# Kernel optimization log

Measured on AMD Instinct MI355X. Metric: run time of the kernel, lower is better.

## Reference

```python
import jax, jax.numpy as jnp
import numpy as np

DIM = 1024
LATENT = 512
HEADS = 16
HEAD_DIM = DIM // HEADS


def setup_inputs() -> dict:
    key = jax.random.key(0)
    ks = jax.random.split(key, 9)
    s = 0.02
    return {
        "x": jax.random.normal(ks[0], (2, 2048, DIM), dtype=jnp.float32),
        "Wq": jax.random.normal(ks[1], (DIM, DIM), dtype=jnp.float32) * s,
        "Wkv": jax.random.normal(ks[2], (DIM, 2 * DIM), dtype=jnp.float32) * s,
        "Wk1": jax.random.normal(ks[3], (DIM, LATENT), dtype=jnp.float32) * s,
        "Wk2": jax.random.normal(ks[4], (LATENT, DIM), dtype=jnp.float32) * s,
        "Wv1": jax.random.normal(ks[5], (DIM, LATENT), dtype=jnp.float32) * s,
        "Wv2": jax.random.normal(ks[6], (LATENT, DIM), dtype=jnp.float32) * s,
        "Wo": jax.random.normal(ks[7], (DIM, DIM), dtype=jnp.float32) * s,
        "bo": jax.random.normal(ks[8], (DIM,), dtype=jnp.float32) * s,
    }


def reference(x, Wq, Wkv, Wk1, Wk2, Wv1, Wv2, Wo, bo):
    b, n, dim = x.shape
    scale = HEAD_DIM ** -0.5
    q = x @ Wq                               # [b, n, dim]
    kv = x @ Wkv                             # [b, n, 2*dim]
    k, v = kv[..., :dim], kv[..., dim:]
    # latent bottleneck MLPs (Linear -> ReLU -> Linear, no bias)
    k = jax.nn.relu(k @ Wk1) @ Wk2           # [b, n, dim]
    v = jax.nn.relu(v @ Wv1) @ Wv2           # [b, n, dim]
    # split heads: [b, n, h*d] -> [b, h, n, d]
    def split_heads(t):
        return t.reshape(b, n, HEADS, HEAD_DIM).transpose(0, 2, 1, 3)
    q = split_heads(q) * scale
    k = split_heads(k)
    v = split_heads(v)
    scores = jnp.einsum('bhid,bhjd->bhij', q, k)   # [b, h, n, n]
    attn = jax.nn.softmax(scores, axis=-1)
    out = jnp.einsum('bhij,bhjd->bhid', attn, v)   # [b, h, n, d]
    out = out.transpose(0, 2, 1, 3).reshape(b, n, dim)
    return out @ Wo + bo
```

## Files before the change

kernel.cpp:

```cpp
#include <hip/hip_runtime.h>
#include <stdint.h>


typedef __attribute__((ext_vector_type(8))) __bf16 bf16x8;
typedef __attribute__((ext_vector_type(4))) float f32x4;

__device__ inline unsigned short f2bfu(float f) {
    __bf16 b = (__bf16)f;
    return __builtin_bit_cast(unsigned short, b);
}

__device__ inline float exp2_fast(float f) {
    return __builtin_amdgcn_exp2f(f);
}

__device__ inline void load_lds16(const void* g, void* l) {
    __builtin_amdgcn_global_load_lds(
        (const __attribute__((address_space(1))) uint32_t*)g,
        (__attribute__((address_space(3))) uint32_t*)l, 16, 0, 0);
}

__device__ inline f32x4 mfma_bf16(bf16x8 a, bf16x8 b, f32x4 c) {
    return __builtin_amdgcn_mfma_f32_16x16x32_bf16(a, b, c, 0, 0, 0);
}

__global__ __launch_bounds__(256) void prep_kernel(
    const float* __restrict__ x, unsigned short* __restrict__ xb,
    const float* __restrict__ Wkv, unsigned short* __restrict__ Wkvb,
    const float* __restrict__ Wq,  const float* __restrict__ Wo,
    const float* __restrict__ Wk1, const float* __restrict__ Wv1,
    const float* __restrict__ Wk2, const float* __restrict__ Wv2,
    unsigned short* __restrict__ WqkvT, unsigned short* __restrict__ WoT,
    unsigned short* __restrict__ Wk1T,  unsigned short* __restrict__ Wv1T,
    unsigned short* __restrict__ Wk2T,  unsigned short* __restrict__ Wv2T,
    float qscale)
{
    __shared__ float tile[64][65];
    int id = blockIdx.x;
    int t = threadIdx.x;

    if (id < 6144) {
        const float* s = (id < 4096) ? x : Wkv;
        unsigned short* d = (id < 4096) ? xb : Wkvb;
        int base = (id < 4096) ? id : (id - 4096);
        int i = (base * 256 + t) * 4;
        float4 v = *(const float4*)&s[i];
        ushort4 o;
        o.x = f2bfu(v.x); o.y = f2bfu(v.y); o.z = f2bfu(v.z); o.w = f2bfu(v.w);
        *(ushort4*)&d[i] = o;
        return;
    }

    int r = id - 6144;
    const float* src; unsigned short* dst; int R, C; float sc; int bx, by;
    if (r < 512) {
        int z = r >> 8; int rr = r & 255; bx = rr & 15; by = rr >> 4;
        src = z ? Wo : Wq; dst = z ? WoT : WqkvT;
        R = 1024; C = 1024; sc = z ? 1.0f : qscale;
    } else if (r < 768) {
        int rr = r - 512; int z = rr >> 7; rr &= 127; bx = rr & 7; by = rr >> 3;
        src = z ? Wv1 : Wk1; dst = z ? Wv1T : Wk1T;
        R = 1024; C = 512; sc = 1.0f;
    } else {
        int rr = r - 768; int z = rr >> 7; rr &= 127; bx = rr & 15; by = rr >> 4;
        src = z ? Wv2 : Wk2; dst = z ? Wv2T : Wk2T;
        R = 512; C = 1024; sc = 1.0f;
    }

    int c0 = bx * 64, r0 = by * 64;
    int col = t & 63, rr4 = t >> 6;
#pragma unroll
    for (int i = 0; i < 16; ++i)
        tile[rr4 + i * 4][col] = src[(size_t)(r0 + rr4 + i * 4) * C + c0 + col];
    __syncthreads();
#pragma unroll
    for (int i = 0; i < 16; ++i) {
        int r2 = rr4 + i * 4;
        dst[(size_t)(c0 + r2) * R + r0 + col] = f2bfu(tile[col][r2] * sc);
    }
}

template<int BN, bool OUTVT = false>
__global__ __launch_bounds__(256) void gemm_bf16_kernel(
    const unsigned short* __restrict__ A0, const unsigned short* __restrict__ A1,
    const unsigned short* __restrict__ B0, const unsigned short* __restrict__ B1,
    void* __restrict__ C0, void* __restrict__ C1,
    int lda, int ldb, int ldc, int K,
    const float* __restrict__ bias, int relu, int out_f32)
{
    const unsigned short* A = blockIdx.z ? A1 : A0;
    const unsigned short* Bt = blockIdx.z ? B1 : B0;
    void* C = blockIdx.z ? C1 : C0;

    constexpr int NI = BN / 32;
    constexpr int AH = 128 * 32;
    constexpr int BH = BN * 32;
    __shared__ unsigned short Als[4 * AH];
    __shared__ unsigned short Bls[4 * BH];
    int t = threadIdx.x;
    int lane = t & 63, w = t >> 6;
    int n0 = blockIdx.x * BN, m0 = blockIdx.y * 128;
    int wm = (w & 1) * 64, wn = (w >> 1) * (BN / 2);
    int lrow = lane & 15, quad = lane >> 4;

    f32x4 acc[4][NI];
    f32x4 z = {0.f, 0.f, 0.f, 0.f};
#pragma unroll
    for (int i = 0; i < 4; ++i)
#pragma unroll
        for (int j = 0; j < NI; ++j) acc[i][j] = z;

    int c0 = t, c1 = t + 256;
    const unsigned short* ag0 = A + (size_t)(m0 + (c0 >> 2)) * lda + (c0 & 3) * 8;
    const unsigned short* ag1 = A + (size_t)(m0 + (c1 >> 2)) * lda + (c1 & 3) * 8;
    const unsigned short* bg0 = Bt + (size_t)(n0 + (c0 >> 2)) * ldb + (c0 & 3) * 8;
    const unsigned short* bg1 = Bt + (size_t)(n0 + ((c1 >> 2) & (BN - 1))) * ldb + (c1 & 3) * 8;

    for (int k0 = 0; k0 < K; k0 += 128) {
        __syncthreads();
#pragma unroll
        for (int h = 0; h < 4; ++h) {
            load_lds16(ag0 + k0 + h * 32, &Als[h * AH + c0 * 8]);
            load_lds16(ag1 + k0 + h * 32, &Als[h * AH + c1 * 8]);
            load_lds16(bg0 + k0 + h * 32, &Bls[h * BH + c0 * 8]);
            if constexpr (BN == 128)
                load_lds16(bg1 + k0 + h * 32, &Bls[h * BH + c1 * 8]);
        }
        __syncthreads();

#pragma unroll
        for (int kk = 0; kk < 4; ++kk) {
            bf16x8 af[4], bfr[NI];
#pragma unroll
            for (int mi = 0; mi < 4; ++mi)
                af[mi] = *(const bf16x8*)&Als[kk * AH + (wm + mi * 16 + lrow) * 32 + quad * 8];
#pragma unroll
            for (int ni = 0; ni < NI; ++ni)
                bfr[ni] = *(const bf16x8*)&Bls[kk * BH + (wn + ni * 16 + lrow) * 32 + quad * 8];
#pragma unroll
            for (int mi = 0; mi < 4; ++mi)
#pragma unroll
                for (int ni = 0; ni < NI; ++ni)
                    acc[mi][ni] = mfma_bf16(af[mi], bfr[ni], acc[mi][ni]);
        }
    }

    if (OUTVT && blockIdx.z) {
        int bb = m0 >> 11;
        int npb = (m0 & 2047) + wm;
        unsigned short* vt = (unsigned short*)C;
#pragma unroll
        for (int mi = 0; mi < 4; ++mi)
#pragma unroll
            for (int ni = 0; ni < NI; ++ni) {
                int col = n0 + wn + ni * 16 + lrow;
                int np = npb + mi * 16 + quad * 4;
                ushort4 o;
                o.x = f2bfu(acc[mi][ni][0]);
                o.y = f2bfu(acc[mi][ni][1]);
                o.z = f2bfu(acc[mi][ni][2]);
                o.w = f2bfu(acc[mi][ni][3]);
                *(ushort4*)&vt[(size_t)(bb * 1024 + col) * 2048 + np] = o;
            }
        return;
    }

#pragma unroll
    for (int mi = 0; mi < 4; ++mi)
#pragma unroll
        for (int ni = 0; ni < NI; ++ni)
#pragma unroll
            for (int r = 0; r < 4; ++r) {
                int row = m0 + wm + mi * 16 + quad * 4 + r;
                int col = n0 + wn + ni * 16 + lrow;
                float v = acc[mi][ni][r];
                if (bias) v += bias[col];
                if (relu == 1 || (relu == 2 && col >= 1024)) v = fmaxf(v, 0.0f);
                if (out_f32) ((float*)C)[(size_t)row * ldc + col] = v;
                else ((unsigned short*)C)[(size_t)row * ldc + col] = f2bfu(v);
            }
}

__global__ __launch_bounds__(256, 2) void flash_mfma_kernel(
    const unsigned short* __restrict__ Q, int ldq,
    const unsigned short* __restrict__ K, int ldk,
    const unsigned short* __restrict__ Vt, unsigned short* __restrict__ O)
{
    __shared__ __align__(16) unsigned short Kls[2][2 * 64 * 32];
    __shared__ __align__(16) unsigned short Vls[2][2 * 64 * 32];
    __shared__ __align__(16) unsigned short Pls[4][2][16 * 64];

    int pbid = blockIdx.x;
    int lbid = (pbid >> 3) + (pbid & 7) * 64;
    int q0 = (lbid & 15) * 128, bh = lbid >> 4;
    int b = bh >> 4, h = bh & 15;
    int t = threadIdx.x;
    int lane = t & 63, w = t >> 6;
    int lrow = lane & 15, quad = lane >> 4;

    bf16x8 qf[2][2];
#pragma unroll
    for (int qb = 0; qb < 2; ++qb) {
        const unsigned short* qrow =
            Q + (size_t)(b * 2048 + q0 + w * 32 + qb * 16 + lrow) * ldq + h * 64;
        qf[qb][0] = *(const bf16x8*)&qrow[quad * 8];
        qf[qb][1] = *(const bf16x8*)&qrow[32 + quad * 8];
    }

    f32x4 z = {0.f, 0.f, 0.f, 0.f};
    f32x4 acco[2][4];
    float m_run[2][4], l_run[2][4];
#pragma unroll
    for (int qb = 0; qb < 2; ++qb)
#pragma unroll
        for (int r = 0; r < 4; ++r) {
            acco[qb][r] = z;
            m_run[qb][r] = -1e30f;
            l_run[qb][r] = 0.f;
        }

    int row4 = t >> 2;
    int seg = (t & 3) * 8;
    const unsigned short* kg = K + (size_t)(b * 2048 + row4) * ldk + h * 64 + seg;
    const unsigned short* vg = Vt + (size_t)(bh * 64 + row4) * 2048 + seg;

    char* pb[2] = { (char*)&Pls[w][0][0], (char*)&Pls[w][1][0] };

    load_lds16(kg,      &Kls[0][t * 8]);
    load_lds16(kg + 32, &Kls[0][2048 + t * 8]);
    load_lds16(vg,      &Vls[0][t * 8]);
    load_lds16(vg + 32, &Vls[0][2048 + t * 8]);
    __syncthreads();

    int cur = 0;
    for (int kt = 0; kt < 2048; kt += 64) {
        if (kt + 64 < 2048) {
            const unsigned short* kgk = kg + (size_t)(kt + 64) * ldk;
            const unsigned short* vgk = vg + kt + 64;
            int nb = cur ^ 1;
            load_lds16(kgk,      &Kls[nb][t * 8]);
            load_lds16(kgk + 32, &Kls[nb][2048 + t * 8]);
            load_lds16(vgk,      &Vls[nb][t * 8]);
            load_lds16(vgk + 32, &Vls[nb][2048 + t * 8]);
        }

        f32x4 s[2][4];
        __builtin_amdgcn_s_setprio(1);
#pragma unroll
        for (int kt8 = 0; kt8 < 4; ++kt8) {
            bf16x8 k0 = *(const bf16x8*)&Kls[cur][(kt8 * 16 + lrow) * 32 + quad * 8];
            bf16x8 k1 = *(const bf16x8*)&Kls[cur][2048 + (kt8 * 16 + lrow) * 32 + quad * 8];
            s[0][kt8] = mfma_bf16(qf[0][0], k0, z);
            s[0][kt8] = mfma_bf16(qf[0][1], k1, s[0][kt8]);
            s[1][kt8] = mfma_bf16(qf[1][0], k0, z);
            s[1][kt8] = mfma_bf16(qf[1][1], k1, s[1][kt8]);
        }
        __builtin_amdgcn_s_setprio(0);

#pragma unroll
        for (int qb = 0; qb < 2; ++qb) {
            float pm[4];
#pragma unroll
            for (int r = 0; r < 4; ++r)
                pm[r] = fmaxf(fmaxf(s[qb][0][r], s[qb][1][r]),
                              fmaxf(s[qb][2][r], s[qb][3][r]));
            bool ok = (pm[0] <= m_run[qb][0] + 8.f) && (pm[1] <= m_run[qb][1] + 8.f)
                   && (pm[2] <= m_run[qb][2] + 8.f) && (pm[3] <= m_run[qb][3] + 8.f);
            if (!__all(ok)) {
#pragma unroll
                for (int r = 0; r < 4; ++r) {
#pragma unroll
                    for (int off = 1; off < 16; off <<= 1)
                        pm[r] = fmaxf(pm[r], __shfl_xor(pm[r], off, 64));
                    float mnew = fmaxf(m_run[qb][r], pm[r]);
                    float al = exp2_fast(m_run[qb][r] - mnew);
                    m_run[qb][r] = mnew;
                    l_run[qb][r] *= al;
#pragma unroll
                    for (int nt = 0; nt < 4; ++nt) acco[qb][nt][r] *= al;
                }
            }
#pragma unroll
            for (int kt8 = 0; kt8 < 4; ++kt8)
#pragma unroll
                for (int r = 0; r < 4; ++r) {
                    float p = exp2_fast(s[qb][kt8][r] - m_run[qb][r]);
                    l_run[qb][r] += p;
                    int row = quad * 4 + r;
                    int boff = (row * 128 + (kt8 * 16 + lrow) * 2) ^ ((row & 7) << 4);
                    *(unsigned short*)(pb[qb] + boff) = f2bfu(p);
                }
        }

        __builtin_amdgcn_s_setprio(1);
#pragma unroll
        for (int ks = 0; ks < 2; ++ks) {
            int rb = (lrow * 128 + ks * 64 + quad * 16) ^ ((lrow & 7) << 4);
            bf16x8 pf0 = *(const bf16x8*)(pb[0] + rb);
            bf16x8 pf1 = *(const bf16x8*)(pb[1] + rb);
#pragma unroll
            for (int nt = 0; nt < 4; ++nt) {
                bf16x8 vf = *(const bf16x8*)&Vls[cur][ks * 2048 + (nt * 16 + lrow) * 32 + quad * 8];
                acco[0][nt] = mfma_bf16(pf0, vf, acco[0][nt]);
                acco[1][nt] = mfma_bf16(pf1, vf, acco[1][nt]);
            }
        }
        __builtin_amdgcn_s_setprio(0);

        __syncthreads();
        cur ^= 1;
    }

#pragma unroll
    for (int qb = 0; qb < 2; ++qb)
#pragma unroll
        for (int r = 0; r < 4; ++r) {
            float lr = l_run[qb][r];
#pragma unroll
            for (int off = 1; off < 16; off <<= 1)
                lr += __shfl_xor(lr, off, 64);
            float rl = 1.0f / lr;
            int row = b * 2048 + q0 + w * 32 + qb * 16 + quad * 4 + r;
#pragma unroll
            for (int nt = 0; nt < 4; ++nt)
                O[(size_t)row * 1024 + h * 64 + nt * 16 + lrow] =
                    f2bfu(acco[qb][nt][r] * rl);
        }
}


extern "C" void kernel_launch(void* const* d_in, const int* in_sizes, int n_in,
                              void* d_out, int out_size, void* d_ws, size_t ws_size,
                              hipStream_t stream) {
    const float* x   = (const float*)d_in[0];
    const float* Wq  = (const float*)d_in[1];
    const float* Wkv = (const float*)d_in[2];
    const float* Wk1 = (const float*)d_in[3];
    const float* Wk2 = (const float*)d_in[4];
    const float* Wv1 = (const float*)d_in[5];
    const float* Wv2 = (const float*)d_in[6];
    const float* Wo  = (const float*)d_in[7];
    const float* bo  = (const float*)d_in[8];
    float* out = (float*)d_out;

    unsigned short* p = (unsigned short*)d_ws;
    unsigned short* xb    = p; p += 4194304;
    unsigned short* Wkvb  = p; p += 2097152;
    unsigned short* WqkvT = p; p += 2097152;
    unsigned short* WoT   = p; p += 1048576;
    unsigned short* Wk1T  = p; p += 524288;
    unsigned short* Wv1T  = p; p += 524288;
    unsigned short* Wk2T  = p; p += 524288;
    unsigned short* Wv2T  = p; p += 524288;
    unsigned short* qkv2  = p; p += 8388608;
    unsigned short* attnb = p; p += 4194304;
    unsigned short* kvo   = p; p += 4194304;
    unsigned short* vtb   = p; p += 4194304;

    dim3 blk(256);
    const float qscale = 0.125f * 1.44269504f;

    prep_kernel<<<7168, blk, 0, stream>>>(
        x, xb, Wkv, Wkvb, Wq, Wo, Wk1, Wv1, Wk2, Wv2,
        WqkvT, WoT, Wk1T, Wv1T, Wk2T, Wv2T, qscale);

    gemm_bf16_kernel<64><<<dim3(16, 4, 2), blk, 0, stream>>>(
        Wk1T, Wv1T, Wkvb, Wkvb + 1024,
        WqkvT + 1024 * 1024, WqkvT + 1536 * 1024,
        1024, 2048, 1024, 1024, nullptr, 0, 0);

    gemm_bf16_kernel<128><<<dim3(16, 32, 1), blk, 0, stream>>>(
        xb, xb, WqkvT, WqkvT, qkv2, qkv2, 1024, 1024, 2048, 1024, nullptr, 2, 0);

    gemm_bf16_kernel<128, true><<<dim3(8, 32, 2), blk, 0, stream>>>(
        qkv2 + 1024, qkv2 + 1536, Wk2T, Wv2T, kvo, vtb,
        2048, 512, 1024, 512, nullptr, 0, 0);

    flash_mfma_kernel<<<dim3(512), blk, 0, stream>>>(qkv2, 2048, kvo, 1024, vtb, attnb);

    gemm_bf16_kernel<64><<<dim3(16, 32, 1), blk, 0, stream>>>(
        attnb, attnb, WoT, WoT, out, out, 1024, 1024, 1024, 1024, bo, 0, 1);
}
```

Baseline: 241.5 us.

## Split flash attention over two KV halves and merge partial results

Each query tile's attention is now split across two blocks, one per half of the key/value sequence, doubling the grid from 512 to 1024 blocks. Each block writes its normalized partial output plus row sum and max, and a new merge kernel combines them with log-sum-exp weights. The launch bound asks for 3 blocks per CU. The aim is better CU occupancy and load balance on the attention kernel, at the cost of an extra kernel launch, extra global traffic for the partial outputs, and another bf16 rounding step.

```diff
diff --git a/kernel.cpp b/kernel.cpp
--- a/kernel.cpp
+++ b/kernel.cpp
@@ -8,6 +8,11 @@
 __device__ inline unsigned short f2bfu(float f) {
     __bf16 b = (__bf16)f;
     return __builtin_bit_cast(unsigned short, b);
+}
+
+__device__ inline float bfu2f(unsigned short u) {
+    unsigned int x = ((unsigned int)u) << 16;
+    return __builtin_bit_cast(float, x);
 }
 
 __device__ inline float exp2_fast(float f) {
@@ -181,22 +186,27 @@
             }
 }
 
-__global__ __launch_bounds__(256, 2) void flash_mfma_kernel(
+__global__ __launch_bounds__(256, 3) void flash_mfma_kernel(
     const unsigned short* __restrict__ Q, int ldq,
     const unsigned short* __restrict__ K, int ldk,
-    const unsigned short* __restrict__ Vt, unsigned short* __restrict__ O)
+    const unsigned short* __restrict__ Vt,
+    unsigned short* __restrict__ Oh, float* __restrict__ lm)
 {
     __shared__ __align__(16) unsigned short Kls[2][2 * 64 * 32];
     __shared__ __align__(16) unsigned short Vls[2][2 * 64 * 32];
     __shared__ __align__(16) unsigned short Pls[4][2][16 * 64];
 
     int pbid = blockIdx.x;
-    int lbid = (pbid >> 3) + (pbid & 7) * 64;
-    int q0 = (lbid & 15) * 128, bh = lbid >> 4;
+    int lbid = (pbid >> 3) + (pbid & 7) * 128;
+    int bh = lbid >> 5;
+    int s5 = lbid & 31;
+    int kvh = s5 & 1;
+    int q0 = (s5 >> 1) * 128;
     int b = bh >> 4, h = bh & 15;
     int t = threadIdx.x;
     int lane = t & 63, w = t >> 6;
     int lrow = lane & 15, quad = lane >> 4;
+    int kt0 = kvh * 1024;
 
     bf16x8 qf[2][2];
 #pragma unroll
@@ -226,15 +236,15 @@
 
     char* pb[2] = { (char*)&Pls[w][0][0], (char*)&Pls[w][1][0] };
 
-    load_lds16(kg,      &Kls[0][t * 8]);
-    load_lds16(kg + 32, &Kls[0][2048 + t * 8]);
-    load_lds16(vg,      &Vls[0][t * 8]);
-    load_lds16(vg + 32, &Vls[0][2048 + t * 8]);
+    load_lds16(kg + (size_t)kt0 * ldk,      &Kls[0][t * 8]);
+    load_lds16(kg + (size_t)kt0 * ldk + 32, &Kls[0][2048 + t * 8]);
+    load_lds16(vg + kt0,      &Vls[0][t * 8]);
+    load_lds16(vg + kt0 + 32, &Vls[0][2048 + t * 8]);
     __syncthreads();
 
     int cur = 0;
-    for (int kt = 0; kt < 2048; kt += 64) {
-        if (kt + 64 < 2048) {
+    for (int kt = kt0; kt < kt0 + 1024; kt += 64) {
+        if (kt + 64 < kt0 + 1024) {
             const unsigned short* kgk = kg + (size_t)(kt + 64) * ldk;
             const unsigned short* vgk = vg + kt + 64;
             int nb = cur ^ 1;
@@ -311,6 +321,8 @@
         cur ^= 1;
     }
 
+    unsigned short* Ob = Oh + (size_t)kvh * 4096 * 1024;
+    float* lmb = lm + (size_t)kvh * 4096 * 16 * 2;
 #pragma unroll
     for (int qb = 0; qb < 2; ++qb)
 #pragma unroll
@@ -323,9 +335,47 @@
             int row = b * 2048 + q0 + w * 32 + qb * 16 + quad * 4 + r;
 #pragma unroll
             for (int nt = 0; nt < 4; ++nt)
-                O[(size_t)row * 1024 + h * 64 + nt * 16 + lrow] =
+                Ob[(size_t)row * 1024 + h * 64 + nt * 16 + lrow] =
                     f2bfu(acco[qb][nt][r] * rl);
-        }
+            if (lrow == 0) {
+                lmb[((size_t)row * 16 + h) * 2 + 0] = lr;
+                lmb[((size_t)row * 16 + h) * 2 + 1] = m_run[qb][r];
+            }
+        }
+}
+
+__global__ __launch_bounds__(256) void merge_kernel(
+    const unsigned short* __restrict__ Oh, const float* __restrict__ lm,
+    unsigned short* __restrict__ attn)
+{
+    int e = blockIdx.x * 256 + threadIdx.x;
+    int base = e * 8;
+    int row = base >> 10, col = base & 1023, h = col >> 6;
+    const float* lm0 = lm + ((size_t)row * 16 + h) * 2;
+    const float* lm1 = lm + ((size_t)(4096 + row) * 16 + h) * 2;
+    float l0 = lm0[0], m0 = lm0[1];
+    float l1 = lm1[0], m1 = lm1[1];
+    float mm = fmaxf(m0, m1);
+    float w0 = l0 * exp2_fast(m0 - mm);
+    float w1 = l1 * exp2_fast(m1 - mm);
+    float rs = 1.0f / (w0 + w1);
+    w0 *= rs; w1 *= rs;
+    const unsigned short* p0 = Oh + (size_t)row * 1024 + col;
+    const unsigned short* p1 = p0 + (size_t)4096 * 1024;
+    ushort4 a0 = *(const ushort4*)p0,       a1 = *(const ushort4*)(p0 + 4);
+    ushort4 b0 = *(const ushort4*)p1,       b1 = *(const ushort4*)(p1 + 4);
+    ushort4 o0, o1;
+    o0.x = f2bfu(w0 * bfu2f(a0.x) + w1 * bfu2f(b0.x));
+    o0.y = f2bfu(w0 * bfu2f(a0.y) + w1 * bfu2f(b0.y));
+    o0.z = f2bfu(w0 * bfu2f(a0.z) + w1 * bfu2f(b0.z));
+    o0.w = f2bfu(w0 * bfu2f(a0.w) + w1 * bfu2f(b0.w));
+    o1.x = f2bfu(w0 * bfu2f(a1.x) + w1 * bfu2f(b1.x));
+    o1.y = f2bfu(w0 * bfu2f(a1.y) + w1 * bfu2f(b1.y));
+    o1.z = f2bfu(w0 * bfu2f(a1.z) + w1 * bfu2f(b1.z));
+    o1.w = f2bfu(w0 * bfu2f(a1.w) + w1 * bfu2f(b1.w));
+    unsigned short* d = attn + (size_t)row * 1024 + col;
+    *(ushort4*)d = o0;
+    *(ushort4*)(d + 4) = o1;
 }
 
 
@@ -356,6 +406,8 @@
     unsigned short* attnb = p; p += 4194304;
     unsigned short* kvo   = p; p += 4194304;
     unsigned short* vtb   = p; p += 4194304;
+    unsigned short* Ohb   = p; p += 8388608;
+    float* lmb = (float*)p; p += 524288;
 
     dim3 blk(256);
     const float qscale = 0.125f * 1.44269504f;
@@ -376,7 +428,9 @@
         qkv2 + 1024, qkv2 + 1536, Wk2T, Wv2T, kvo, vtb,
         2048, 512, 1024, 512, nullptr, 0, 0);
 
-    flash_mfma_kernel<<<dim3(512), blk, 0, stream>>>(qkv2, 2048, kvo, 1024, vtb, attnb);
+    flash_mfma_kernel<<<dim3(1024), blk, 0, stream>>>(
+        qkv2, 2048, kvo, 1024, vtb, Ohb, lmb);
+    merge_kernel<<<dim3(2048), blk, 0, stream>>>(Ohb, lmb, attnb);
 
     gemm_bf16_kernel<64><<<dim3(16, 32, 1), blk, 0, stream>>>(
         attnb, attnb, WoT, WoT, out, out, 1024, 1024, 1024, 1024, bo, 0, 1);
```

New measurement: 250.6 us. 3.8% more time.
